# Kernel tuning notes

Measured on AMD Instinct MI355X. Metric: run time of the kernel, lower is better.

Reference implementation:

```python
import jax, jax.numpy as jnp
import numpy as np

B, C, O, H, W = 16, 256, 256, 64, 64
T_DIM, E, K = 512, 4, 3


def setup_inputs() -> dict:
    key = jax.random.key(0)
    ks = jax.random.split(key, 12)
    def rn(k, shape, s=0.02):
        return jax.random.normal(k, shape, jnp.float32) * s
    return dict(
        x=jax.random.normal(ks[0], (B, C, H, W), jnp.float32),
        time_emb=jax.random.normal(ks[1], (B, T_DIM), jnp.float32),
        Wq=rn(ks[2], (C, T_DIM)), bq=jnp.zeros((C,), jnp.float32),
        Wk=rn(ks[3], (C, C)), bk=jnp.zeros((C,), jnp.float32),
        Wv=rn(ks[4], (C, C)), bv=jnp.zeros((C,), jnp.float32),
        Wm1=rn(ks[5], (C // 4, C)), bm1=jnp.zeros((C // 4,), jnp.float32),
        Wm2=rn(ks[6], (C, C // 4)), bm2=jnp.zeros((C,), jnp.float32),
        Wc=rn(ks[7], (E, C)), bc=jnp.zeros((E,), jnp.float32),
        expert_w=rn(ks[8], (E, O, C, K, K), s=0.05),  # [E, O, C_in/groups, K, K]
        expert_b=rn(ks[9], (E, O), s=0.05),
    )


def reference(x, time_emb, Wq, bq, Wk, bk, Wv, bv, Wm1, bm1, Wm2, bm2, Wc, bc, expert_w, expert_b):
    # --- router (eval mode: no gating noise) ---
    pooled = x.mean(axis=(2, 3))                      # [B, C] == avg_pool over full HxW
    q = time_emb @ Wq.T + bq                          # [B, C]
    k = pooled @ Wk.T + bk                            # [B, C]
    attn = jax.nn.sigmoid(q * k)
    v = pooled @ Wv.T + bv
    x_att = v * attn
    h = jax.nn.gelu(x_att @ Wm1.T + bm1, approximate=False) @ Wm2.T + bm2
    x_mix = x_att + h
    logits = x_mix @ Wc.T + bc                        # [B, E]
    rw = jnp.tanh(logits)                             # routing weights [B, E]

    # --- per-sample expert-weight mixing ---
    w_eff = jnp.einsum('be,eoihw->boihw', rw, expert_w)  # [B, O, C, K, K]
    b_eff = rw @ expert_b                                 # [B, O]

    # --- per-sample conv (equivalent to groups=B trick) ---
    def conv_one(xb, wb):
        # xb: [C, H, W], wb: [O, C, K, K]
        return jax.lax.conv_general_dilated(
            xb[None], wb, window_strides=(1, 1), padding=[(1, 1), (1, 1)],
            dimension_numbers=('NCHW', 'OIHW', 'NCHW'))[0]

    out = jax.vmap(conv_one)(x, w_eff)                 # [B, O, H, W]
    return out + b_eff[:, :, None, None]
```

## Files before the change

### kernel.cpp

```cpp
#include <hip/hip_runtime.h>

typedef __bf16 bf16x8 __attribute__((ext_vector_type(8)));
typedef float f32x4 __attribute__((ext_vector_type(4)));

__device__ __forceinline__ unsigned short f2bf(float f) {
  union { float f; unsigned int u; } v;
  v.f = f;
  unsigned int r = v.u + 0x7FFFu + ((v.u >> 16) & 1u);
  return (unsigned short)(r >> 16);
}

__device__ __forceinline__ void load_lds16(const void* g, void* l) {
  __builtin_amdgcn_global_load_lds(
      (__attribute__((address_space(1))) void*)(void*)g,
      (__attribute__((address_space(3))) void*)l, 16, 0, 0);
}

__global__ void transpose_kernel(const float* __restrict__ x, unsigned short* __restrict__ xTpad,
                                 float* __restrict__ part) {
  int bid = blockIdx.x;
  int b = bid / 66, hp = bid % 66;
  unsigned short* rowbase = xTpad + ((size_t)(b * 66 + hp)) * 66 * 256;
  int t = threadIdx.x;
  if (hp == 0 || hp == 65) {
    uint4 z = make_uint4(0u, 0u, 0u, 0u);
    for (int i = t; i < 2112; i += 256) ((uint4*)rowbase)[i] = z;
    return;
  }
  int h = hp - 1;
  __shared__ unsigned short lds[64][264];
  __shared__ float psum[256];
  const float* xb = x + ((size_t)b * 256 * 64 + h) * 64;
  int lane = t & 63;
  #pragma unroll
  for (int g = 0; g < 16; ++g) {
    int c = g * 16 + (t >> 4);
    int w0 = (t & 15) * 4;
    float4 v = *(const float4*)&xb[(size_t)c * 4096 + w0];
    lds[w0 + 0][c] = f2bf(v.x);
    lds[w0 + 1][c] = f2bf(v.y);
    lds[w0 + 2][c] = f2bf(v.z);
    lds[w0 + 3][c] = f2bf(v.w);
    float s = v.x + v.y + v.z + v.w;
    s += __shfl_xor(s, 1); s += __shfl_xor(s, 2);
    s += __shfl_xor(s, 4); s += __shfl_xor(s, 8);
    if ((lane & 15) == 0) psum[c] = s;
  }
  __syncthreads();
  #pragma unroll
  for (int p = 0; p < 8; ++p) {
    int w = p * 8 + (t >> 5);
    int seg = t & 31;
    uint4 u = *(const uint4*)&lds[w][seg * 8];
    *(uint4*)&rowbase[(w + 1) * 256 + seg * 8] = u;
  }
  if (t < 64) {
    uint4 z = make_uint4(0u, 0u, 0u, 0u);
    int row = (t >> 5) ? 65 : 0;
    *(uint4*)&rowbase[row * 256 + (t & 31) * 8] = z;
  }
  if (t < 256) part[((size_t)b * 64 + h) * 256 + t] = psum[t];
}

__global__ void router_kernel(
    const float* __restrict__ time_emb, const float* __restrict__ part,
    const float* __restrict__ Wq, const float* __restrict__ bq,
    const float* __restrict__ Wk, const float* __restrict__ bk,
    const float* __restrict__ Wv, const float* __restrict__ bv,
    const float* __restrict__ Wm1, const float* __restrict__ bm1,
    const float* __restrict__ Wm2, const float* __restrict__ bm2,
    const float* __restrict__ Wc, const float* __restrict__ bc,
    const float* __restrict__ expert_b,
    float* __restrict__ rw_out, float* __restrict__ beff_out) {
  int b = blockIdx.x, tid = threadIdx.x;
  int t = tid & 255;
  __shared__ float te[512], pl[256], qs[256], xa[256], m1s[64], xms[256], rws[4];
  te[tid] = time_emb[b * 512 + tid];
  if (tid < 256) {
    float s = 0.f;
    const float* pp = part + (size_t)b * 16384 + tid;
    for (int hh = 0; hh < 64; ++hh) s += pp[hh * 256];
    pl[tid] = s * (1.0f / 4096.0f);
  }
  __syncthreads();
  if (tid < 256) {
    float q = bq[t];
    const float4* wq4 = (const float4*)(Wq + (size_t)t * 512);
    #pragma unroll 4
    for (int i = 0; i < 128; ++i) {
      float4 w4 = wq4[i];
      q += w4.x * te[i*4] + w4.y * te[i*4+1] + w4.z * te[i*4+2] + w4.w * te[i*4+3];
    }
    qs[t] = q;
  } else {
    float k = bk[t], v = bv[t];
    const float4* wk4 = (const float4*)(Wk + (size_t)t * 256);
    const float4* wv4 = (const float4*)(Wv + (size_t)t * 256);
    #pragma unroll 4
    for (int i = 0; i < 64; ++i) {
      float4 a4 = wk4[i], b4 = wv4[i];
      float p0 = pl[i*4], p1 = pl[i*4+1], p2 = pl[i*4+2], p3 = pl[i*4+3];
      k += a4.x * p0 + a4.y * p1 + a4.z * p2 + a4.w * p3;
      v += b4.x * p0 + b4.y * p1 + b4.z * p2 + b4.w * p3;
    }
    xa[t] = k;
    xms[t] = v;
  }
  __syncthreads();
  if (tid < 256) {
    float k = xa[t], v = xms[t];
    float attn = 1.0f / (1.0f + expf(-(qs[t] * k)));
    qs[t] = v * attn;
  }
  __syncthreads();
  if (tid < 64) {
    float s = bm1[tid];
    const float4* w1 = (const float4*)(Wm1 + (size_t)tid * 256);
    #pragma unroll 4
    for (int i = 0; i < 64; ++i) {
      float4 w4 = w1[i];
      s += w4.x * qs[i*4] + w4.y * qs[i*4+1] + w4.z * qs[i*4+2] + w4.w * qs[i*4+3];
    }
    m1s[tid] = 0.5f * s * (1.0f + erff(s * 0.7071067811865476f));
  }
  __syncthreads();
  if (tid < 256) {
    float hsum = bm2[t];
    const float* w2 = Wm2 + (size_t)t * 64;
    for (int j = 0; j < 64; ++j) hsum += m1s[j] * w2[j];
    xms[t] = qs[t] + hsum;
  }
  __syncthreads();
  if (tid < 4) {
    float s = bc[tid];
    const float* wc = Wc + (size_t)tid * 256;
    for (int i = 0; i < 256; ++i) s += xms[i] * wc[i];
    float r = tanhf(s);
    rws[tid] = r;
    rw_out[b * 4 + tid] = r;
  }
  __syncthreads();
  if (tid < 256) {
    float be = 0.f;
    #pragma unroll
    for (int e = 0; e < 4; ++e) be += rws[e] * expert_b[e * 256 + t];
    beff_out[b * 256 + t] = be;
  }
}

__global__ void wmix_kernel(const float* __restrict__ ew, const float* __restrict__ rw,
                            unsigned short* __restrict__ wmixT) {
  int ob = blockIdx.x % 16, kr = blockIdx.x / 16;
  int t = threadIdx.x;
  int lm = t & 15, kcl = t >> 4;
  int kc = kr * 16 + kcl;
  int tap = kc >> 5;
  int c0 = (kc & 31) * 8;
  __shared__ float rsh[64];
  if (t < 64) rsh[t] = rw[t];
  int o = ob * 16 + lm;
  float wv[4][8];
  #pragma unroll
  for (int e = 0; e < 4; ++e) {
    const float* s = ew + (((size_t)e * 256 + o) * 256 + c0) * 9 + tap;
    #pragma unroll
    for (int j = 0; j < 8; ++j) wv[e][j] = s[j * 9];
  }
  __syncthreads();
  for (int b = 0; b < 16; ++b) {
    float r0 = rsh[b*4], r1 = rsh[b*4+1], r2 = rsh[b*4+2], r3 = rsh[b*4+3];
    unsigned short tmp[8];
    #pragma unroll
    for (int j = 0; j < 8; ++j) {
      float m = r0*wv[0][j] + r1*wv[1][j] + r2*wv[2][j] + r3*wv[3][j];
      tmp[j] = f2bf(m);
    }
    *(uint4*)&wmixT[(((size_t)(b*16 + ob)*288 + kc)*128) + lm*8] = *(uint4*)tmp;
  }
}

__global__ __launch_bounds__(512, 2) void conv_kernel(
    const unsigned short* __restrict__ xT, const unsigned short* __restrict__ wmixT,
    const float* __restrict__ beff, float* __restrict__ out) {
  __shared__ unsigned short Bs[2][16384];
  int bid = blockIdx.x;
  int b = ((bid & 7) << 1) | ((bid >> 7) & 1);
  int nt = (bid >> 3) & 15;
  int h0 = nt << 2;
  int tid = threadIdx.x;
  int wid = tid >> 6, lane = tid & 63;
  int lm = lane & 15, lg = lane >> 4;
  int wm = wid >> 1, wn = wid & 1;

  const unsigned short* xTb = xT + (size_t)b * 66 * 66 * 256;
  const unsigned short* wmA = wmixT + (size_t)(b * 16 + wm * 4) * 288 * 128 + lane * 8;

  int lr = lane >> 3;
  int slot_g = (lane & 7) ^ lr;
  int b_lane = lr * 256 + slot_g * 8;

  int sw0 = ((0 + lg) ^ (lm & 7)) * 8;
  int sw1 = ((4 + lg) ^ (lm & 7)) * 8;

  auto stB = [&](int buf, int kh, int cc, int kw, int q) {
    const unsigned short* src =
        xTb + (size_t)((h0 + q + kh) * 66 + wid * 8 + kw) * 256 + cc * 64 + b_lane;
    load_lds16(src, &Bs[buf][(q * 64 + wid * 8) * 64]);
  };

  f32x4 acc[4][8];
  #pragma unroll
  for (int mf = 0; mf < 4; ++mf)
    #pragma unroll
    for (int nf = 0; nf < 8; ++nf)
      acc[mf][nf] = (f32x4){0.f, 0.f, 0.f, 0.f};

  bf16x8 Ae[4][2], Ao[4][2];

  stB(0, 0, 0, 0, 0); stB(0, 0, 0, 0, 1); stB(0, 0, 0, 0, 2); stB(0, 0, 0, 0, 3);
  __builtin_amdgcn_sched_barrier(0);
  #pragma unroll
  for (int mf = 0; mf < 4; ++mf)
    #pragma unroll
    for (int kk = 0; kk < 2; ++kk)
      Ae[mf][kk] = *(const bf16x8*)(wmA + (size_t)(mf * 288 + kk * 4) * 128);
  asm volatile("s_waitcnt vmcnt(8)" ::: "memory");
  __builtin_amdgcn_s_barrier();

  auto tile_body = [&](int t, int buf, bf16x8 (&Acur)[4][2], bf16x8 (&Anext)[4][2])
      __attribute__((always_inline)) {
    bool st = (t < 35);
    if (st) {
      int tn = t + 1;
      int khn = tn / 12, rn = tn % 12, ccn = rn / 3, kwn = rn % 3;
      stB(buf ^ 1, khn, ccn, kwn, 0); stB(buf ^ 1, khn, ccn, kwn, 1);
      stB(buf ^ 1, khn, ccn, kwn, 2); stB(buf ^ 1, khn, ccn, kwn, 3);
      __builtin_amdgcn_sched_barrier(0);
      int kbase = (khn * 3 + kwn) * 32 + ccn * 8;
      #pragma unroll
      for (int mf = 0; mf < 4; ++mf)
        #pragma unroll
        for (int kk = 0; kk < 2; ++kk)
          Anext[mf][kk] = *(const bf16x8*)(wmA + (size_t)(mf * 288 + kbase + kk * 4) * 128);
    }
    #pragma unroll
    for (int nf = 0; nf < 8; ++nf) {
      bf16x8 b0 = *(const bf16x8*)&Bs[buf][(wn * 128 + nf * 16 + lm) * 64 + sw0];
      bf16x8 b1 = *(const bf16x8*)&Bs[buf][(wn * 128 + nf * 16 + lm) * 64 + sw1];
      #pragma unroll
      for (int mf = 0; mf < 4; ++mf) {
        acc[mf][nf] = __builtin_amdgcn_mfma_f32_16x16x32_bf16(Acur[mf][0], b0, acc[mf][nf], 0, 0, 0);
        acc[mf][nf] = __builtin_amdgcn_mfma_f32_16x16x32_bf16(Acur[mf][1], b1, acc[mf][nf], 0, 0, 0);
      }
    }
    if (st) {
      asm volatile("s_waitcnt vmcnt(8)" ::: "memory");
      __builtin_amdgcn_s_barrier();
    }
  };

  for (int i = 0; i < 18; ++i) {
    tile_body(2 * i, 0, Ae, Ao);
    tile_body(2 * i + 1, 1, Ao, Ae);
  }

  #pragma unroll
  for (int mf = 0; mf < 4; ++mf) {
    int o = wm * 64 + mf * 16 + lg * 4;
    float be0 = beff[b * 256 + o + 0];
    float be1 = beff[b * 256 + o + 1];
    float be2 = beff[b * 256 + o + 2];
    float be3 = beff[b * 256 + o + 3];
    #pragma unroll
    for (int nf = 0; nf < 8; ++nf) {
      int n = wn * 128 + nf * 16 + lm;
      int hh = h0 + (n >> 6), w = n & 63;
      float* op = out + (((size_t)(b * 256 + o)) * 64 + hh) * 64 + w;
      op[0]            = acc[mf][nf][0] + be0;
      op[4096]         = acc[mf][nf][1] + be1;
      op[2 * 4096]     = acc[mf][nf][2] + be2;
      op[3 * 4096]     = acc[mf][nf][3] + be3;
    }
  }
}

extern "C" void kernel_launch(void* const* d_in, const int* in_sizes, int n_in,
                              void* d_out, int out_size, void* d_ws, size_t ws_size,
                              hipStream_t stream) {
  const float* x        = (const float*)d_in[0];
  const float* time_emb = (const float*)d_in[1];
  const float* Wq = (const float*)d_in[2];
  const float* bq = (const float*)d_in[3];
  const float* Wk = (const float*)d_in[4];
  const float* bk = (const float*)d_in[5];
  const float* Wv = (const float*)d_in[6];
  const float* bv = (const float*)d_in[7];
  const float* Wm1 = (const float*)d_in[8];
  const float* bm1 = (const float*)d_in[9];
  const float* Wm2 = (const float*)d_in[10];
  const float* bm2 = (const float*)d_in[11];
  const float* Wc = (const float*)d_in[12];
  const float* bc = (const float*)d_in[13];
  const float* expert_w = (const float*)d_in[14];
  const float* expert_b = (const float*)d_in[15];
  float* out = (float*)d_out;

  char* ws = (char*)d_ws;
  float* rw   = (float*)(ws + 0);
  float* beff = (float*)(ws + 1024);
  float* part = (float*)(ws + 20480);
  unsigned short* xTpad  = (unsigned short*)(ws + 1069056);
  unsigned short* wmixT  = (unsigned short*)(ws + 1069056 + 35684352);

  transpose_kernel<<<1056, 256, 0, stream>>>(x, xTpad, part);
  router_kernel<<<16, 512, 0, stream>>>(time_emb, part, Wq, bq, Wk, bk, Wv, bv,
                                        Wm1, bm1, Wm2, bm2, Wc, bc, expert_b, rw, beff);
  wmix_kernel<<<288, 256, 0, stream>>>(expert_w, rw, wmixT);
  conv_kernel<<<256, 512, 0, stream>>>(xTpad, wmixT, beff, out);
}
```

Baseline: 162.6 us.

## Shrink conv tiles to two rows per block and reorganize mixed weight layout

Result: slower. 168.7 us (+3.7%).

```diff
diff --git a/kernel.cpp b/kernel.cpp
--- a/kernel.cpp
+++ b/kernel.cpp
@@ -149,51 +149,49 @@
 }
 
 __global__ void wmix_kernel(const float* __restrict__ ew, const float* __restrict__ rw,
-                            unsigned short* __restrict__ wmixT) {
-  int ob = blockIdx.x % 16, kr = blockIdx.x / 16;
-  int t = threadIdx.x;
-  int lm = t & 15, kcl = t >> 4;
-  int kc = kr * 16 + kcl;
-  int tap = kc >> 5;
-  int c0 = (kc & 31) * 8;
+                            unsigned short* __restrict__ wmix) {
+  int o = blockIdx.x, t = threadIdx.x;
+  __shared__ float lew[4][2304];
   __shared__ float rsh[64];
   if (t < 64) rsh[t] = rw[t];
-  int o = ob * 16 + lm;
-  float wv[4][8];
   #pragma unroll
   for (int e = 0; e < 4; ++e) {
-    const float* s = ew + (((size_t)e * 256 + o) * 256 + c0) * 9 + tap;
-    #pragma unroll
-    for (int j = 0; j < 8; ++j) wv[e][j] = s[j * 9];
-  }
-  __syncthreads();
+    const float* s = ew + ((size_t)e * 256 + o) * 2304;
+    #pragma unroll
+    for (int j = 0; j < 9; ++j) lew[e][j * 256 + t] = s[j * 256 + t];
+  }
+  __syncthreads();
+  float wv[4][9];
+  #pragma unroll
+  for (int e = 0; e < 4; ++e)
+    #pragma unroll
+    for (int tt = 0; tt < 9; ++tt) wv[e][tt] = lew[e][t * 9 + tt];
   for (int b = 0; b < 16; ++b) {
     float r0 = rsh[b*4], r1 = rsh[b*4+1], r2 = rsh[b*4+2], r3 = rsh[b*4+3];
-    unsigned short tmp[8];
-    #pragma unroll
-    for (int j = 0; j < 8; ++j) {
-      float m = r0*wv[0][j] + r1*wv[1][j] + r2*wv[2][j] + r3*wv[3][j];
-      tmp[j] = f2bf(m);
-    }
-    *(uint4*)&wmixT[(((size_t)(b*16 + ob)*288 + kc)*128) + lm*8] = *(uint4*)tmp;
-  }
-}
-
-__global__ __launch_bounds__(512, 2) void conv_kernel(
-    const unsigned short* __restrict__ xT, const unsigned short* __restrict__ wmixT,
+    unsigned short* wo = wmix + ((size_t)b * 256 + o) * 2304 + t;
+    #pragma unroll
+    for (int tt = 0; tt < 9; ++tt) {
+      float m = r0 * wv[0][tt] + r1 * wv[1][tt] + r2 * wv[2][tt] + r3 * wv[3][tt];
+      wo[tt * 256] = f2bf(m);
+    }
+  }
+}
+
+__global__ __launch_bounds__(256, 2) void conv_kernel(
+    const unsigned short* __restrict__ xT, const unsigned short* __restrict__ wmix,
     const float* __restrict__ beff, float* __restrict__ out) {
-  __shared__ unsigned short Bs[2][16384];
+  __shared__ unsigned short Bs[2][8192];
   int bid = blockIdx.x;
-  int b = ((bid & 7) << 1) | ((bid >> 7) & 1);
-  int nt = (bid >> 3) & 15;
-  int h0 = nt << 2;
+  int b = ((bid & 7) << 1) | ((bid >> 8) & 1);
+  int nt = (bid >> 3) & 31;
+  int h0 = nt << 1;
   int tid = threadIdx.x;
   int wid = tid >> 6, lane = tid & 63;
   int lm = lane & 15, lg = lane >> 4;
-  int wm = wid >> 1, wn = wid & 1;
 
   const unsigned short* xTb = xT + (size_t)b * 66 * 66 * 256;
-  const unsigned short* wmA = wmixT + (size_t)(b * 16 + wm * 4) * 288 * 128 + lane * 8;
+  const unsigned short* wmb = wmix + (size_t)b * 256 * 2304;
+  const unsigned short* wmA = wmb + (size_t)(wid * 64 + lm) * 2304 + lg * 8;
 
   int lr = lane >> 3;
   int slot_g = (lane & 7) ^ lr;
@@ -202,10 +200,12 @@
   int sw0 = ((0 + lg) ^ (lm & 7)) * 8;
   int sw1 = ((4 + lg) ^ (lm & 7)) * 8;
 
-  auto stB = [&](int buf, int kh, int cc, int kw, int q) {
+  auto stB = [&](int buf, int kh, int cc, int kw, int j) {
+    int r0 = wid * 32 + j * 8;
+    int q = r0 >> 6, w0 = r0 & 63;
     const unsigned short* src =
-        xTb + (size_t)((h0 + q + kh) * 66 + wid * 8 + kw) * 256 + cc * 64 + b_lane;
-    load_lds16(src, &Bs[buf][(q * 64 + wid * 8) * 64]);
+        xTb + (size_t)((h0 + q + kh) * 66 + w0 + kw) * 256 + cc * 64 + b_lane;
+    load_lds16(src, &Bs[buf][r0 * 64]);
   };
 
   f32x4 acc[4][8];
@@ -223,7 +223,7 @@
   for (int mf = 0; mf < 4; ++mf)
     #pragma unroll
     for (int kk = 0; kk < 2; ++kk)
-      Ae[mf][kk] = *(const bf16x8*)(wmA + (size_t)(mf * 288 + kk * 4) * 128);
+      Ae[mf][kk] = *(const bf16x8*)(wmA + (size_t)(mf * 16) * 2304 + kk * 32);
   asm volatile("s_waitcnt vmcnt(8)" ::: "memory");
   __builtin_amdgcn_s_barrier();
 
@@ -236,17 +236,17 @@
       stB(buf ^ 1, khn, ccn, kwn, 0); stB(buf ^ 1, khn, ccn, kwn, 1);
       stB(buf ^ 1, khn, ccn, kwn, 2); stB(buf ^ 1, khn, ccn, kwn, 3);
       __builtin_amdgcn_sched_barrier(0);
-      int kbase = (khn * 3 + kwn) * 32 + ccn * 8;
+      int kbase = (khn * 3 + kwn) * 256 + ccn * 64;
       #pragma unroll
       for (int mf = 0; mf < 4; ++mf)
         #pragma unroll
         for (int kk = 0; kk < 2; ++kk)
-          Anext[mf][kk] = *(const bf16x8*)(wmA + (size_t)(mf * 288 + kbase + kk * 4) * 128);
+          Anext[mf][kk] = *(const bf16x8*)(wmA + (size_t)(mf * 16) * 2304 + kbase + kk * 32);
     }
     #pragma unroll
     for (int nf = 0; nf < 8; ++nf) {
-      bf16x8 b0 = *(const bf16x8*)&Bs[buf][(wn * 128 + nf * 16 + lm) * 64 + sw0];
-      bf16x8 b1 = *(const bf16x8*)&Bs[buf][(wn * 128 + nf * 16 + lm) * 64 + sw1];
+      bf16x8 b0 = *(const bf16x8*)&Bs[buf][(nf * 16 + lm) * 64 + sw0];
+      bf16x8 b1 = *(const bf16x8*)&Bs[buf][(nf * 16 + lm) * 64 + sw1];
       #pragma unroll
       for (int mf = 0; mf < 4; ++mf) {
         acc[mf][nf] = __builtin_amdgcn_mfma_f32_16x16x32_bf16(Acur[mf][0], b0, acc[mf][nf], 0, 0, 0);
@@ -266,14 +266,14 @@
 
   #pragma unroll
   for (int mf = 0; mf < 4; ++mf) {
-    int o = wm * 64 + mf * 16 + lg * 4;
+    int o = wid * 64 + mf * 16 + lg * 4;
     float be0 = beff[b * 256 + o + 0];
     float be1 = beff[b * 256 + o + 1];
     float be2 = beff[b * 256 + o + 2];
     float be3 = beff[b * 256 + o + 3];
     #pragma unroll
     for (int nf = 0; nf < 8; ++nf) {
-      int n = wn * 128 + nf * 16 + lm;
+      int n = nf * 16 + lm;
       int hh = h0 + (n >> 6), w = n & 63;
       float* op = out + (((size_t)(b * 256 + o)) * 64 + hh) * 64 + w;
       op[0]            = acc[mf][nf][0] + be0;
@@ -309,12 +309,12 @@
   float* rw   = (float*)(ws + 0);
   float* beff = (float*)(ws + 1024);
   float* part = (float*)(ws + 20480);
-  unsigned short* xTpad  = (unsigned short*)(ws + 1069056);
-  unsigned short* wmixT  = (unsigned short*)(ws + 1069056 + 35684352);
+  unsigned short* xTpad = (unsigned short*)(ws + 1069056);
+  unsigned short* wmix  = (unsigned short*)(ws + 1069056 + 35684352);
 
   transpose_kernel<<<1056, 256, 0, stream>>>(x, xTpad, part);
   router_kernel<<<16, 512, 0, stream>>>(time_emb, part, Wq, bq, Wk, bk, Wv, bv,
                                         Wm1, bm1, Wm2, bm2, Wc, bc, expert_b, rw, beff);
-  wmix_kernel<<<288, 256, 0, stream>>>(expert_w, rw, wmixT);
-  conv_kernel<<<256, 512, 0, stream>>>(xTpad, wmixT, beff, out);
-}
+  wmix_kernel<<<256, 256, 0, stream>>>(expert_w, rw, wmix);
+  conv_kernel<<<512, 256, 0, stream>>>(xTpad, wmix, beff, out);
+}
```

## Restructure expert-weight mixing to stage coalesced loads through LDS per sample

Applied to the files above, without the earlier changes.

New measurement: 155.1 us (median of 2 runs). 4.6% less time.

```diff
diff --git a/kernel.cpp b/kernel.cpp
--- a/kernel.cpp
+++ b/kernel.cpp
@@ -148,35 +148,37 @@
   }
 }
 
-__global__ void wmix_kernel(const float* __restrict__ ew, const float* __restrict__ rw,
-                            unsigned short* __restrict__ wmixT) {
-  int ob = blockIdx.x % 16, kr = blockIdx.x / 16;
+__global__ __launch_bounds__(256, 1) void wmixT_kernel(
+    const float* __restrict__ ew, const float* __restrict__ rw,
+    unsigned short* __restrict__ wmixT) {
+  int b = blockIdx.x >> 4, ob = blockIdx.x & 15;
   int t = threadIdx.x;
-  int lm = t & 15, kcl = t >> 4;
-  int kc = kr * 16 + kcl;
-  int tap = kc >> 5;
-  int c0 = (kc & 31) * 8;
-  __shared__ float rsh[64];
-  if (t < 64) rsh[t] = rw[t];
-  int o = ob * 16 + lm;
-  float wv[4][8];
-  #pragma unroll
-  for (int e = 0; e < 4; ++e) {
-    const float* s = ew + (((size_t)e * 256 + o) * 256 + c0) * 9 + tap;
-    #pragma unroll
-    for (int j = 0; j < 8; ++j) wv[e][j] = s[j * 9];
-  }
-  __syncthreads();
-  for (int b = 0; b < 16; ++b) {
-    float r0 = rsh[b*4], r1 = rsh[b*4+1], r2 = rsh[b*4+2], r3 = rsh[b*4+3];
-    unsigned short tmp[8];
-    #pragma unroll
-    for (int j = 0; j < 8; ++j) {
-      float m = r0*wv[0][j] + r1*wv[1][j] + r2*wv[2][j] + r3*wv[3][j];
-      tmp[j] = f2bf(m);
-    }
-    *(uint4*)&wmixT[(((size_t)(b*16 + ob)*288 + kc)*128) + lm*8] = *(uint4*)tmp;
-  }
+  __shared__ float lew[4][2304];
+  __shared__ unsigned short obuf[288 * 128];
+  float r0 = rw[b * 4 + 0], r1 = rw[b * 4 + 1], r2 = rw[b * 4 + 2], r3 = rw[b * 4 + 3];
+  for (int op = 0; op < 16; ++op) {
+    int o = ob * 16 + op;
+    if (op) __syncthreads();
+    #pragma unroll
+    for (int e = 0; e < 4; ++e) {
+      const float* s = ew + ((size_t)e * 256 + o) * 2304;
+      #pragma unroll
+      for (int j = 0; j < 9; ++j) lew[e][j * 256 + t] = s[j * 256 + t];
+    }
+    __syncthreads();
+    int base = (t >> 3) * 128 + op * 8 + (t & 7);
+    #pragma unroll
+    for (int tt = 0; tt < 9; ++tt) {
+      float m = r0 * lew[0][t * 9 + tt] + r1 * lew[1][t * 9 + tt] +
+                r2 * lew[2][t * 9 + tt] + r3 * lew[3][t * 9 + tt];
+      obuf[tt * 32 * 128 + base] = f2bf(m);
+    }
+  }
+  __syncthreads();
+  uint4* dst = (uint4*)(wmixT + (size_t)(b * 16 + ob) * 288 * 128);
+  const uint4* src = (const uint4*)obuf;
+  #pragma unroll
+  for (int i = 0; i < 18; ++i) dst[i * 256 + t] = src[i * 256 + t];
 }
 
 __global__ __launch_bounds__(512, 2) void conv_kernel(
@@ -309,12 +311,12 @@
   float* rw   = (float*)(ws + 0);
   float* beff = (float*)(ws + 1024);
   float* part = (float*)(ws + 20480);
-  unsigned short* xTpad  = (unsigned short*)(ws + 1069056);
-  unsigned short* wmixT  = (unsigned short*)(ws + 1069056 + 35684352);
+  unsigned short* xTpad = (unsigned short*)(ws + 1069056);
+  unsigned short* wmixT = (unsigned short*)(ws + 1069056 + 35684352);
 
   transpose_kernel<<<1056, 256, 0, stream>>>(x, xTpad, part);
   router_kernel<<<16, 512, 0, stream>>>(time_emb, part, Wq, bq, Wk, bk, Wv, bv,
                                         Wm1, bm1, Wm2, bm2, Wc, bc, expert_b, rw, beff);
-  wmix_kernel<<<288, 256, 0, stream>>>(expert_w, rw, wmixT);
+  wmixT_kernel<<<256, 256, 0, stream>>>(expert_w, rw, wmixT);
   conv_kernel<<<256, 512, 0, stream>>>(xTpad, wmixT, beff, out);
 }
```
